# Kernel optimization log

Hardware: AMD Instinct MI355X
Metric: run time of the kernel (lower is better)

Reference implementation:

```python
import jax, jax.numpy as jnp
import numpy as np

D_MODEL = 1024
N_HEADS = 16
D_KV = 64
B, S = 2, 2048


def setup_inputs() -> dict:
    key = jax.random.key(0)
    ks = jax.random.split(key, 7)
    scale = 1.0 / np.sqrt(D_MODEL)
    return {
        "query": jax.random.normal(ks[0], (B, S, D_MODEL), jnp.float32),
        "key": jax.random.normal(ks[1], (B, S, D_MODEL), jnp.float32),
        "value": jax.random.normal(ks[2], (B, S, D_MODEL), jnp.float32),
        "mask": jnp.zeros((B, 1, 1, S), jnp.float32),
        "Wq": jax.random.normal(ks[3], (D_MODEL, N_HEADS * D_KV), jnp.float32) * scale,
        "Wk": jax.random.normal(ks[4], (D_MODEL, N_HEADS * D_KV), jnp.float32) * scale,
        "Wv": jax.random.normal(ks[5], (D_MODEL, N_HEADS * D_KV), jnp.float32) * scale,
        "Wo": jax.random.normal(ks[6], (N_HEADS * D_KV, D_MODEL), jnp.float32) * scale,
    }


def _split_heads(x):
    b, s, _ = x.shape
    return x.reshape(b, s, N_HEADS, D_KV).transpose(0, 2, 1, 3)  # [B,H,S,Dk]


def reference(query, key, value, mask, Wq, Wk, Wv, Wo):
    q = _split_heads(query @ Wq)
    k = _split_heads(key @ Wk)
    v = _split_heads(value @ Wv)
    scores = jnp.einsum("bhqd,bhkd->bhqk", q, k) / jnp.sqrt(
        jnp.asarray(D_KV, scores_dtype := q.dtype)
    )
    scores = scores + mask
    attn = jax.nn.softmax(scores, axis=-1)  # dropout_rate=0 -> identity
    ctx = jnp.einsum("bhqk,bhkd->bhqd", attn, v)
    ctx = ctx.transpose(0, 2, 1, 3).reshape(query.shape[0], -1, N_HEADS * D_KV)
    hidden = ctx @ Wo
    return hidden
```

## Files before the change

### kernel.cpp

```cpp
#include <hip/hip_runtime.h>
#include <hip/hip_bf16.h>
#include <stdint.h>

typedef __bf16 bf16;
typedef __bf16 bf16x8 __attribute__((ext_vector_type(8)));
typedef __bf16 bf16x4 __attribute__((ext_vector_type(4)));
typedef float  f32x4  __attribute__((ext_vector_type(4)));
typedef float  f32x16 __attribute__((ext_vector_type(16)));

#define S_LEN  2048
#define NH     16
#define DKV    64
#define DMODEL 1024
#define LOG2E  1.4426950408889634f

#define SBAR()       __builtin_amdgcn_s_barrier()
#define SFENCE()     __builtin_amdgcn_sched_barrier(0)
#define WAIT_VM(N)   asm volatile("s_waitcnt vmcnt(" #N ")" ::: "memory")
#define WAIT_LGKM0() asm volatile("s_waitcnt lgkmcnt(0)" ::: "memory")

__device__ __forceinline__ void async_load16(const void* g, void* l) {
  __builtin_amdgcn_global_load_lds(
      (const __attribute__((address_space(1))) uint32_t*)(uintptr_t)g,
      (__attribute__((address_space(3))) uint32_t*)(uintptr_t)l,
      16, 0, 0);
}

__global__ void transpose_w(const float* __restrict__ W0, const float* __restrict__ W1,
                            const float* __restrict__ W2, const float* __restrict__ W3,
                            bf16* __restrict__ T0, bf16* __restrict__ T1,
                            bf16* __restrict__ T2, bf16* __restrict__ T3)
{
  int z = blockIdx.z;
  const float* W = (z == 0) ? W0 : (z == 1) ? W1 : (z == 2) ? W2 : W3;
  bf16* T = (z == 0) ? T0 : (z == 1) ? T1 : (z == 2) ? T2 : T3;
  __shared__ float tile[64][65];
  int n0 = blockIdx.x * 64, k0 = blockIdx.y * 64;
  int tid = threadIdx.x;

  int c4 = (tid & 15) * 4;
  int rr = tid >> 4;
  for (int g = 0; g < 4; ++g) {
    int k = g * 16 + rr;
    f32x4 v = *(const f32x4*)(W + (size_t)(k0 + k) * DMODEL + n0 + c4);
    tile[k][c4] = v[0]; tile[k][c4 + 1] = v[1];
    tile[k][c4 + 2] = v[2]; tile[k][c4 + 3] = v[3];
  }
  __syncthreads();

  int kc = tid & 7, rn2 = tid >> 3;
  for (int pass = 0; pass < 2; ++pass) {
    int rn = pass * 32 + rn2;
    bf16x8 o;
    for (int w = 0; w < 8; ++w) o[w] = (bf16)tile[kc * 8 + w][rn];
    *(bf16x8*)(T + (size_t)(n0 + rn) * DMODEL + k0 + kc * 8) = o;
  }
}

__global__ __launch_bounds__(256) void gemm_qkv(
    const float* __restrict__ Aq, const float* __restrict__ Ak, const float* __restrict__ Av,
    const bf16* __restrict__ Bq, const bf16* __restrict__ Bk, const bf16* __restrict__ Bv,
    bf16* __restrict__ Cq, bf16* __restrict__ Ck, bf16* __restrict__ Cv)
{
  __shared__ __align__(16) char smem[49152];
  bf16* As  = (bf16*)smem;
  bf16* Bs0 = (bf16*)(smem + 16384);
  bf16* Bs1 = (bf16*)(smem + 32768);
  bf16* Ls  = (bf16*)smem;

  const int z = blockIdx.z;
  const float* A = (z == 0) ? Aq : (z == 1) ? Ak : Av;
  const bf16* Bt = (z == 0) ? Bq : (z == 1) ? Bk : Bv;
  bf16* C        = (z == 0) ? Cq : (z == 1) ? Ck : Cv;

  const int m0 = blockIdx.x * 128;
  const int n0 = blockIdx.y * 128;
  const int tid = threadIdx.x;
  const int lane = tid & 63;
  const int wave = tid >> 6;
  const int wm = (wave >> 1) * 64;
  const int wn = (wave & 1) * 64;
  const int row = lane & 15;
  const int quad = lane >> 4;

  f32x4 acc[4][4];
  for (int i = 0; i < 4; ++i)
    for (int j = 0; j < 4; ++j) acc[i][j] = (f32x4){0.f, 0.f, 0.f, 0.f};

  const int arc = tid & 7;
  const int arr = tid >> 3;
  const float* Ap0 = A + (size_t)(m0 +  0 + arr) * DMODEL + arc * 8;
  const float* Ap1 = A + (size_t)(m0 + 32 + arr) * DMODEL + arc * 8;
  const float* Ap2 = A + (size_t)(m0 + 64 + arr) * DMODEL + arc * 8;
  const float* Ap3 = A + (size_t)(m0 + 96 + arr) * DMODEL + arc * 8;

  auto stageB = [&](int kt, bf16* Bsel) {
    const int kk = kt << 6;
    for (int j = 0; j < 4; ++j) {
      int base = j * 256 + wave * 64;
      int idx = base + lane;
      int r = idx >> 3;
      int cc = (idx & 7) ^ (r & 7);
      async_load16(Bt + (size_t)(n0 + r) * DMODEL + kk + cc * 8,
                   (char*)Bsel + (size_t)base * 16);
    }
  };

  f32x4 av[4][2];
  av[0][0] = *(const f32x4*)(Ap0); av[0][1] = *(const f32x4*)(Ap0 + 4);
  av[1][0] = *(const f32x4*)(Ap1); av[1][1] = *(const f32x4*)(Ap1 + 4);
  av[2][0] = *(const f32x4*)(Ap2); av[2][1] = *(const f32x4*)(Ap2 + 4);
  av[3][0] = *(const f32x4*)(Ap3); av[3][1] = *(const f32x4*)(Ap3 + 4);
  SFENCE();
  stageB(0, Bs0);
  SFENCE();

  for (int kt = 0; kt < 16; ++kt) {
    bf16* Bcur = (kt & 1) ? Bs1 : Bs0;
    bf16* Bnxt = (kt & 1) ? Bs0 : Bs1;
    if (kt < 15) stageB(kt + 1, Bnxt);
#pragma unroll
    for (int g = 0; g < 4; ++g) {
      bf16x8 o;
      for (int w = 0; w < 4; ++w) { o[w] = (bf16)av[g][0][w]; o[w + 4] = (bf16)av[g][1][w]; }
      int r = g * 32 + arr;
      *(bf16x8*)(As + r * 64 + ((arc ^ (arr & 7)) << 3)) = o;
    }
    if (kt < 15) {
      const int kn = (kt + 1) << 6;
      av[0][0] = *(const f32x4*)(Ap0 + kn); av[0][1] = *(const f32x4*)(Ap0 + kn + 4);
      av[1][0] = *(const f32x4*)(Ap1 + kn); av[1][1] = *(const f32x4*)(Ap1 + kn + 4);
      av[2][0] = *(const f32x4*)(Ap2 + kn); av[2][1] = *(const f32x4*)(Ap2 + kn + 4);
      av[3][0] = *(const f32x4*)(Ap3 + kn); av[3][1] = *(const f32x4*)(Ap3 + kn + 4);
    }
    SFENCE();
    if (kt < 15) { WAIT_VM(12); }
    else         { WAIT_VM(0); }
    WAIT_LGKM0();
    SBAR();
    SFENCE();
    for (int ks = 0; ks < 2; ++ks) {
      bf16x8 af[4], bfr[4];
      for (int i = 0; i < 4; ++i) {
        int rr = wm + i * 16 + row;
        af[i] = *(const bf16x8*)(As + rr * 64 + (((quad + ks * 4) ^ (rr & 7)) << 3));
      }
      for (int j = 0; j < 4; ++j) {
        int rr = wn + j * 16 + row;
        bfr[j] = *(const bf16x8*)(Bcur + rr * 64 + (((quad + ks * 4) ^ (rr & 7)) << 3));
      }
      for (int i = 0; i < 4; ++i)
        for (int j = 0; j < 4; ++j)
          acc[i][j] = __builtin_amdgcn_mfma_f32_16x16x32_bf16(af[i], bfr[j], acc[i][j], 0, 0, 0);
    }
    SFENCE();
    SBAR();
  }

  if (z != 2) {
    const int bq = m0 >> 11;
    __syncthreads();
    for (int i = 0; i < 4; ++i)
      for (int j = 0; j < 4; ++j)
        for (int r = 0; r < 4; ++r)
          Ls[(wm + i * 16 + quad * 4 + r) * 132 + wn + j * 16 + row] = (bf16)acc[i][j][r];
    __syncthreads();
    for (int u = 0; u < 8; ++u) {
      int cc = u * 256 + tid;
      int rloc = cc >> 4, c8 = (cc & 15) * 8;
      int s = (m0 + rloc) & 2047;
      int gn = n0 + c8;
      int h = gn >> 6, d = gn & 63;
      bf16x8 val = *(const bf16x8*)(Ls + rloc * 132 + c8);
      *(bf16x8*)(C + (((size_t)(bq * NH + h)) * S_LEN + s) * DKV + d) = val;
    }
  } else {
    for (int i = 0; i < 4; ++i)
      for (int j = 0; j < 4; ++j) {
        int gm = m0 + wm + i * 16 + quad * 4;
        int gn = n0 + wn + j * 16 + row;
        int b = gm >> 11, s = gm & 2047;
        int h = gn >> 6,  d = gn & 63;
        int bh = b * NH + h;
        int tile = s >> 6, kb = (s & 63) >> 2;
        int half = (kb >> 1) & 1;
        int p = (kb & 1) + ((kb >> 2) & 1) * 2 + (kb >> 3) * 4;
        bf16x4 t;
        for (int r = 0; r < 4; ++r) t[r] = (bf16)acc[i][j][r];
        *(bf16x4*)(C + ((((size_t)bh * 32 + tile) * 8 + p) * 64 + d) * 8 + half * 4) = t;
      }
  }
}

__global__ __launch_bounds__(256, 4) void attn_kernel(
    const bf16* __restrict__ Qh, const bf16* __restrict__ Kh, const bf16* __restrict__ Vperm,
    const float* __restrict__ mask, bf16* __restrict__ Opart, float* __restrict__ Lpart)
{
  __shared__ __align__(16) bf16 Ks[2][64 * 64];
  __shared__ __align__(16) bf16 Vts[2][64 * 64];
  __shared__ __align__(16) float masks2[2][64];

  const int bh = blockIdx.x;
  const int b = bh >> 4;
  const int q0 = blockIdx.y * 128;
  const int zh = blockIdx.z;
  const int tid = threadIdx.x;
  const int lane = tid & 63;
  const int wave = tid >> 6;
  const int ln = lane & 31;
  const int hi = lane >> 5;
  const float SC2 = 0.125f * LOG2E;

  const int qg = q0 + wave * 32 + ln;
  bf16x8 qf[4];
  {
    const bf16* qrow = Qh + ((size_t)bh * S_LEN + qg) * DKV;
    for (int c = 0; c < 4; ++c)
      qf[c] = *(const bf16x8*)(qrow + c * 16 + hi * 8);
  }

  auto stage = [&](int it, int buf) {
    const int kv0 = zh * 1024 + it * 64;
    float mval = 0.f;
    if (tid < 64) mval = mask[b * S_LEN + kv0 + tid];
    const bf16* vtile = Vperm + ((size_t)bh * 32 + (kv0 >> 6)) * 4096;
    for (int j = 0; j < 2; ++j) {
      int base = j * 256 + wave * 64;
      int idx = base + lane;
      int r = idx >> 3;
      int cc = (idx & 7) ^ (r & 7);
      async_load16(Kh + ((size_t)bh * S_LEN + kv0 + r) * DKV + cc * 8,
                   (char*)Ks[buf] + (size_t)base * 16);
      async_load16(vtile + (size_t)idx * 8,
                   (char*)Vts[buf] + (size_t)base * 16);
    }
    if (tid < 64) masks2[buf][tid] = mval * LOG2E;
  };

  f32x16 O[2];
  for (int nb = 0; nb < 2; ++nb)
    for (int i = 0; i < 16; ++i) O[nb][i] = 0.f;
  float lsum = 0.f;

  stage(0, 0);

  for (int it = 0; it < 16; ++it) {
    const int cur = it & 1;
    if (it < 15) stage(it + 1, cur ^ 1);
    SFENCE();
    if (it < 15) { WAIT_VM(4); }
    else         { WAIT_VM(0); }
    WAIT_LGKM0();
    SBAR();
    SFENCE();

    f32x16 Sm[2];
    for (int i = 0; i < 16; ++i) { Sm[0][i] = 0.f; Sm[1][i] = 0.f; }
    for (int c = 0; c < 4; ++c) {
      bf16x8 k0 = *(const bf16x8*)(Ks[cur] + ln * 64        + (((2 * c + hi) ^ (ln & 7)) << 3));
      bf16x8 k1 = *(const bf16x8*)(Ks[cur] + (32 + ln) * 64 + (((2 * c + hi) ^ (ln & 7)) << 3));
      Sm[0] = __builtin_amdgcn_mfma_f32_32x32x16_bf16(k0, qf[c], Sm[0], 0, 0, 0);
      Sm[1] = __builtin_amdgcn_mfma_f32_32x32x16_bf16(k1, qf[c], Sm[1], 0, 0, 0);
    }

    for (int cg = 0; cg < 4; ++cg) {
      int mb = cg >> 1, g = cg & 1;
      int koff = 32 * mb + 16 * g + 4 * hi;
      f32x4 mklo = *(const f32x4*)(&masks2[cur][koff]);
      f32x4 mkhi = *(const f32x4*)(&masks2[cur][koff + 8]);
      bf16x8 ap;
      float ls0 = 0.f;
      for (int u = 0; u < 4; ++u) {
        float p = __builtin_amdgcn_exp2f(Sm[mb][g * 8 + u] * SC2 + mklo[u]);
        ls0 += p; ap[u] = (bf16)p;
      }
      for (int u = 0; u < 4; ++u) {
        float p = __builtin_amdgcn_exp2f(Sm[mb][g * 8 + 4 + u] * SC2 + mkhi[u]);
        ls0 += p; ap[4 + u] = (bf16)p;
      }
      lsum += ls0;
      int p = hi + 2 * g + 4 * mb;
      for (int nb = 0; nb < 2; ++nb) {
        int d = nb * 32 + ln;
        bf16x8 bv = *(const bf16x8*)(Vts[cur] + ((size_t)p * 64 + d) * 8);
        O[nb] = __builtin_amdgcn_mfma_f32_32x32x16_bf16(ap, bv, O[nb], 0, 0, 0);
      }
    }
    SFENCE();
    SBAR();
  }

  float lt = lsum + __shfl_xor(lsum, 32, 64);
  if (lane < 32)
    Lpart[((size_t)zh * 32 + bh) * S_LEN + q0 + wave * 32 + ln] = lt;

  bf16* ob = Opart + (((size_t)zh * 32 + bh) * S_LEN) * DKV;
  for (int g = 0; g < 4; ++g)
    for (int nb = 0; nb < 2; ++nb)
      for (int j = 0; j < 4; ++j) {
        int qrow = q0 + wave * 32 + j + 8 * g + 4 * hi;
        ob[(size_t)qrow * DKV + nb * 32 + ln] = (bf16)O[nb][g * 4 + j];
      }
}

__global__ __launch_bounds__(256) void gemm_out(
    const bf16* __restrict__ Opart, const float* __restrict__ Lpart,
    const bf16* __restrict__ Wot, float* __restrict__ Cout)
{
  __shared__ __align__(16) bf16 As[64 * 64];
  __shared__ __align__(16) bf16 Bs[2][128 * 64];
  __shared__ float rinv[NH * 64];

  const int m0 = blockIdx.x * 64;
  const int n0 = blockIdx.y * 128;
  const int tid = threadIdx.x;
  const int lane = tid & 63;
  const int wave = tid >> 6;
  const int wm = (wave >> 1) * 32;
  const int wn = (wave & 1) * 64;
  const int row = lane & 15;
  const int quad = lane >> 4;
  const int b = m0 >> 11;
  const int s0 = m0 & 2047;

  for (int u = 0; u < 4; ++u) {
    int idx = u * 256 + tid;
    int h = idx >> 6, r = idx & 63;
    float l = Lpart[(size_t)(b * NH + h) * S_LEN + s0 + r]
            + Lpart[(size_t)(32 + b * NH + h) * S_LEN + s0 + r];
    rinv[idx] = 1.0f / l;
  }
  SFENCE();

  f32x4 acc[2][4];
  for (int i = 0; i < 2; ++i)
    for (int j = 0; j < 4; ++j) acc[i][j] = (f32x4){0.f, 0.f, 0.f, 0.f};

  const int arc = tid & 7;
  const int arr = tid >> 3;
  const size_t HSTEP = (size_t)S_LEN * DKV;
  const size_t ZSTEP = (size_t)32 * S_LEN * DKV;
  const bf16* Oa = Opart + ((size_t)(b * NH) * S_LEN + s0 + arr) * DKV + arc * 8;
  const bf16* Ob = Oa + (size_t)32 * DKV;

  auto stageB = [&](int kt, int buf) {
    for (int j = 0; j < 4; ++j) {
      int base = j * 256 + wave * 64;
      int idx = base + lane;
      int r = idx >> 3;
      int cc = (idx & 7) ^ (r & 7);
      async_load16(Wot + (size_t)(n0 + r) * DMODEL + kt * 64 + cc * 8,
                   (char*)Bs[buf] + (size_t)base * 16);
    }
  };

  bf16x8 h00 = *(const bf16x8*)(Oa);
  bf16x8 h01 = *(const bf16x8*)(Oa + ZSTEP);
  bf16x8 h10 = *(const bf16x8*)(Ob);
  bf16x8 h11 = *(const bf16x8*)(Ob + ZSTEP);
  SFENCE();
  stageB(0, 0);
  SFENCE();
  WAIT_LGKM0();
  SBAR();

  for (int kt = 0; kt < 16; ++kt) {
    const int cur = kt & 1;
    if (kt < 15) stageB(kt + 1, cur ^ 1);
    {
      float rv  = rinv[kt * 64 + arr];
      float rv2 = rinv[kt * 64 + 32 + arr];
      bf16x8 o;
      for (int w = 0; w < 8; ++w)
        o[w] = (bf16)(((float)h00[w] + (float)h01[w]) * rv);
      *(bf16x8*)(As + arr * 64 + ((arc ^ (arr & 7)) << 3)) = o;
      for (int w = 0; w < 8; ++w)
        o[w] = (bf16)(((float)h10[w] + (float)h11[w]) * rv2);
      *(bf16x8*)(As + (32 + arr) * 64 + ((arc ^ (arr & 7)) << 3)) = o;
    }
    if (kt < 15) {
      const size_t off = (size_t)(kt + 1) * HSTEP;
      h00 = *(const bf16x8*)(Oa + off);
      h01 = *(const bf16x8*)(Oa + off + ZSTEP);
      h10 = *(const bf16x8*)(Ob + off);
      h11 = *(const bf16x8*)(Ob + off + ZSTEP);
    }
    SFENCE();
    if (kt < 15) { WAIT_VM(8); }
    else         { WAIT_VM(0); }
    WAIT_LGKM0();
    SBAR();
    SFENCE();
    for (int ks = 0; ks < 2; ++ks) {
      bf16x8 af[2], bfr[4];
      for (int i = 0; i < 2; ++i) {
        int rr = wm + i * 16 + row;
        af[i] = *(const bf16x8*)(As + rr * 64 + (((quad + ks * 4) ^ (rr & 7)) << 3));
      }
      for (int j = 0; j < 4; ++j) {
        int rr = wn + j * 16 + row;
        bfr[j] = *(const bf16x8*)(Bs[cur] + rr * 64 + (((quad + ks * 4) ^ (rr & 7)) << 3));
      }
      for (int i = 0; i < 2; ++i)
        for (int j = 0; j < 4; ++j)
          acc[i][j] = __builtin_amdgcn_mfma_f32_16x16x32_bf16(af[i], bfr[j], acc[i][j], 0, 0, 0);
    }
    SFENCE();
    SBAR();
  }

  for (int i = 0; i < 2; ++i)
    for (int j = 0; j < 4; ++j)
      for (int r = 0; r < 4; ++r) {
        int gm = m0 + wm + i * 16 + quad * 4 + r;
        int gn = n0 + wn + j * 16 + row;
        Cout[(size_t)gm * DMODEL + gn] = acc[i][j][r];
      }
}

extern "C" void kernel_launch(void* const* d_in, const int* in_sizes, int n_in,
                              void* d_out, int out_size, void* d_ws, size_t ws_size,
                              hipStream_t stream)
{
  const float* query = (const float*)d_in[0];
  const float* key_  = (const float*)d_in[1];
  const float* value = (const float*)d_in[2];
  const float* mask  = (const float*)d_in[3];
  const float* Wq = (const float*)d_in[4];
  const float* Wk = (const float*)d_in[5];
  const float* Wv = (const float*)d_in[6];
  const float* Wo = (const float*)d_in[7];

  char* ws = (char*)d_ws;
  const size_t MB = (size_t)1 << 20;
  bf16* qh    = (bf16*)(ws + 0 * MB);
  bf16* kh    = (bf16*)(ws + 8 * MB);
  bf16* vperm = (bf16*)(ws + 16 * MB);
  bf16* wot   = (bf16*)(ws + 24 * MB);
  bf16* Opart = (bf16*)(ws + 26 * MB);
  bf16* wqt   = (bf16*)(ws + 26 * MB);
  bf16* wkt   = (bf16*)(ws + 28 * MB);
  bf16* wvt   = (bf16*)(ws + 30 * MB);
  float* Lpart = (float*)(ws + 58 * MB);

  transpose_w<<<dim3(16, 16, 4), 256, 0, stream>>>(Wq, Wk, Wv, Wo, wqt, wkt, wvt, wot);
  gemm_qkv<<<dim3(32, 8, 3), 256, 0, stream>>>(query, key_, value, wqt, wkt, wvt,
                                               qh, kh, vperm);
  attn_kernel<<<dim3(32, 16, 2), 256, 0, stream>>>(qh, kh, vperm, mask, Opart, Lpart);
  gemm_out<<<dim3(64, 8), 256, 0, stream>>>(Opart, Lpart, wot, (float*)d_out);
}
```

Baseline: 209.6 us.

## Pre-convert QKV activations to bf16 in a fused prep kernel and simplify GEMM staging

The weight-transpose kernel now also converts the fp32 query/key/value activations to bf16 in a separate grid slice, writing them to new workspace buffers. The QKV GEMM then loads A tiles with async global-to-LDS copies like B, using a single LDS buffer with a full wait each k-step instead of double buffering B and converting fp32 A in registers. This removes the per-block fp32 A conversion and halves A read bytes inside the GEMM, but adds an extra activation round trip through memory and loses the load/compute overlap in the GEMM loop. Separately, s_setprio raises wave priority around the MFMA sections in the attention kernel.

```diff
diff --git a/kernel.cpp b/kernel.cpp
--- a/kernel.cpp
+++ b/kernel.cpp
@@ -26,50 +26,66 @@
       16, 0, 0);
 }
 
-__global__ void transpose_w(const float* __restrict__ W0, const float* __restrict__ W1,
-                            const float* __restrict__ W2, const float* __restrict__ W3,
-                            bf16* __restrict__ T0, bf16* __restrict__ T1,
-                            bf16* __restrict__ T2, bf16* __restrict__ T3)
+__global__ void prep(const float* __restrict__ W0, const float* __restrict__ W1,
+                     const float* __restrict__ W2, const float* __restrict__ W3,
+                     const float* __restrict__ Aq, const float* __restrict__ Ak,
+                     const float* __restrict__ Av,
+                     bf16* __restrict__ T0, bf16* __restrict__ T1,
+                     bf16* __restrict__ T2, bf16* __restrict__ T3,
+                     bf16* __restrict__ Qb, bf16* __restrict__ Kb, bf16* __restrict__ Vb)
 {
-  int z = blockIdx.z;
-  const float* W = (z == 0) ? W0 : (z == 1) ? W1 : (z == 2) ? W2 : W3;
-  bf16* T = (z == 0) ? T0 : (z == 1) ? T1 : (z == 2) ? T2 : T3;
-  __shared__ float tile[64][65];
-  int n0 = blockIdx.x * 64, k0 = blockIdx.y * 64;
-  int tid = threadIdx.x;
-
-  int c4 = (tid & 15) * 4;
-  int rr = tid >> 4;
-  for (int g = 0; g < 4; ++g) {
-    int k = g * 16 + rr;
-    f32x4 v = *(const f32x4*)(W + (size_t)(k0 + k) * DMODEL + n0 + c4);
-    tile[k][c4] = v[0]; tile[k][c4 + 1] = v[1];
-    tile[k][c4 + 2] = v[2]; tile[k][c4 + 3] = v[3];
-  }
-  __syncthreads();
-
-  int kc = tid & 7, rn2 = tid >> 3;
-  for (int pass = 0; pass < 2; ++pass) {
-    int rn = pass * 32 + rn2;
-    bf16x8 o;
-    for (int w = 0; w < 8; ++w) o[w] = (bf16)tile[kc * 8 + w][rn];
-    *(bf16x8*)(T + (size_t)(n0 + rn) * DMODEL + k0 + kc * 8) = o;
+  const int z = blockIdx.z;
+  const int tid = threadIdx.x;
+  if (z < 4) {
+    if (blockIdx.x >= 16) return;
+    const float* W = (z == 0) ? W0 : (z == 1) ? W1 : (z == 2) ? W2 : W3;
+    bf16* T = (z == 0) ? T0 : (z == 1) ? T1 : (z == 2) ? T2 : T3;
+    __shared__ float tile[64][65];
+    int n0 = blockIdx.x * 64, k0 = blockIdx.y * 64;
+    int c4 = (tid & 15) * 4;
+    int rr = tid >> 4;
+    for (int g = 0; g < 4; ++g) {
+      int k = g * 16 + rr;
+      f32x4 v = *(const f32x4*)(W + (size_t)(k0 + k) * DMODEL + n0 + c4);
+      tile[k][c4] = v[0]; tile[k][c4 + 1] = v[1];
+      tile[k][c4 + 2] = v[2]; tile[k][c4 + 3] = v[3];
+    }
+    __syncthreads();
+    int kc = tid & 7, rn2 = tid >> 3;
+    for (int pass = 0; pass < 2; ++pass) {
+      int rn = pass * 32 + rn2;
+      bf16x8 o;
+      for (int w = 0; w < 8; ++w) o[w] = (bf16)tile[kc * 8 + w][rn];
+      *(bf16x8*)(T + (size_t)(n0 + rn) * DMODEL + k0 + kc * 8) = o;
+    }
+  } else {
+    const float* S = (z == 4) ? Aq : (z == 5) ? Ak : Av;
+    bf16* D = (z == 4) ? Qb : (z == 5) ? Kb : Vb;
+    size_t base = (((size_t)blockIdx.y * 64 + blockIdx.x) * 256 + tid) * 16;
+    f32x4 v0 = *(const f32x4*)(S + base);
+    f32x4 v1 = *(const f32x4*)(S + base + 4);
+    f32x4 v2 = *(const f32x4*)(S + base + 8);
+    f32x4 v3 = *(const f32x4*)(S + base + 12);
+    bf16x8 o0, o1;
+    for (int w = 0; w < 4; ++w) { o0[w] = (bf16)v0[w]; o0[w + 4] = (bf16)v1[w]; }
+    for (int w = 0; w < 4; ++w) { o1[w] = (bf16)v2[w]; o1[w + 4] = (bf16)v3[w]; }
+    *(bf16x8*)(D + base) = o0;
+    *(bf16x8*)(D + base + 8) = o1;
   }
 }
 
 __global__ __launch_bounds__(256) void gemm_qkv(
-    const float* __restrict__ Aq, const float* __restrict__ Ak, const float* __restrict__ Av,
+    const bf16* __restrict__ Aq, const bf16* __restrict__ Ak, const bf16* __restrict__ Av,
     const bf16* __restrict__ Bq, const bf16* __restrict__ Bk, const bf16* __restrict__ Bv,
     bf16* __restrict__ Cq, bf16* __restrict__ Ck, bf16* __restrict__ Cv)
 {
-  __shared__ __align__(16) char smem[49152];
-  bf16* As  = (bf16*)smem;
-  bf16* Bs0 = (bf16*)(smem + 16384);
-  bf16* Bs1 = (bf16*)(smem + 32768);
-  bf16* Ls  = (bf16*)smem;
+  __shared__ __align__(16) char smem[33792];
+  bf16* As = (bf16*)smem;
+  bf16* Bs = (bf16*)(smem + 16384);
+  bf16* Ls = (bf16*)smem;
 
   const int z = blockIdx.z;
-  const float* A = (z == 0) ? Aq : (z == 1) ? Ak : Av;
+  const bf16* A  = (z == 0) ? Aq : (z == 1) ? Ak : Av;
   const bf16* Bt = (z == 0) ? Bq : (z == 1) ? Bk : Bv;
   bf16* C        = (z == 0) ? Cq : (z == 1) ? Ck : Cv;
 
@@ -87,58 +103,20 @@
   for (int i = 0; i < 4; ++i)
     for (int j = 0; j < 4; ++j) acc[i][j] = (f32x4){0.f, 0.f, 0.f, 0.f};
 
-  const int arc = tid & 7;
-  const int arr = tid >> 3;
-  const float* Ap0 = A + (size_t)(m0 +  0 + arr) * DMODEL + arc * 8;
-  const float* Ap1 = A + (size_t)(m0 + 32 + arr) * DMODEL + arc * 8;
-  const float* Ap2 = A + (size_t)(m0 + 64 + arr) * DMODEL + arc * 8;
-  const float* Ap3 = A + (size_t)(m0 + 96 + arr) * DMODEL + arc * 8;
-
-  auto stageB = [&](int kt, bf16* Bsel) {
+  for (int kt = 0; kt < 16; ++kt) {
     const int kk = kt << 6;
     for (int j = 0; j < 4; ++j) {
       int base = j * 256 + wave * 64;
       int idx = base + lane;
       int r = idx >> 3;
       int cc = (idx & 7) ^ (r & 7);
+      async_load16(A  + (size_t)(m0 + r) * DMODEL + kk + cc * 8,
+                   (char*)As + (size_t)base * 16);
       async_load16(Bt + (size_t)(n0 + r) * DMODEL + kk + cc * 8,
-                   (char*)Bsel + (size_t)base * 16);
-    }
-  };
-
-  f32x4 av[4][2];
-  av[0][0] = *(const f32x4*)(Ap0); av[0][1] = *(const f32x4*)(Ap0 + 4);
-  av[1][0] = *(const f32x4*)(Ap1); av[1][1] = *(const f32x4*)(Ap1 + 4);
-  av[2][0] = *(const f32x4*)(Ap2); av[2][1] = *(const f32x4*)(Ap2 + 4);
-  av[3][0] = *(const f32x4*)(Ap3); av[3][1] = *(const f32x4*)(Ap3 + 4);
-  SFENCE();
-  stageB(0, Bs0);
-  SFENCE();
-
-  for (int kt = 0; kt < 16; ++kt) {
-    bf16* Bcur = (kt & 1) ? Bs1 : Bs0;
-    bf16* Bnxt = (kt & 1) ? Bs0 : Bs1;
-    if (kt < 15) stageB(kt + 1, Bnxt);
-#pragma unroll
-    for (int g = 0; g < 4; ++g) {
-      bf16x8 o;
-      for (int w = 0; w < 4; ++w) { o[w] = (bf16)av[g][0][w]; o[w + 4] = (bf16)av[g][1][w]; }
-      int r = g * 32 + arr;
-      *(bf16x8*)(As + r * 64 + ((arc ^ (arr & 7)) << 3)) = o;
-    }
-    if (kt < 15) {
-      const int kn = (kt + 1) << 6;
-      av[0][0] = *(const f32x4*)(Ap0 + kn); av[0][1] = *(const f32x4*)(Ap0 + kn + 4);
-      av[1][0] = *(const f32x4*)(Ap1 + kn); av[1][1] = *(const f32x4*)(Ap1 + kn + 4);
-      av[2][0] = *(const f32x4*)(Ap2 + kn); av[2][1] = *(const f32x4*)(Ap2 + kn + 4);
-      av[3][0] = *(const f32x4*)(Ap3 + kn); av[3][1] = *(const f32x4*)(Ap3 + kn + 4);
-    }
-    SFENCE();
-    if (kt < 15) { WAIT_VM(12); }
-    else         { WAIT_VM(0); }
-    WAIT_LGKM0();
-    SBAR();
-    SFENCE();
+                   (char*)Bs + (size_t)base * 16);
+    }
+    WAIT_VM(0);
+    SBAR();
     for (int ks = 0; ks < 2; ++ks) {
       bf16x8 af[4], bfr[4];
       for (int i = 0; i < 4; ++i) {
@@ -147,13 +125,12 @@
       }
       for (int j = 0; j < 4; ++j) {
         int rr = wn + j * 16 + row;
-        bfr[j] = *(const bf16x8*)(Bcur + rr * 64 + (((quad + ks * 4) ^ (rr & 7)) << 3));
+        bfr[j] = *(const bf16x8*)(Bs + rr * 64 + (((quad + ks * 4) ^ (rr & 7)) << 3));
       }
       for (int i = 0; i < 4; ++i)
         for (int j = 0; j < 4; ++j)
           acc[i][j] = __builtin_amdgcn_mfma_f32_16x16x32_bf16(af[i], bfr[j], acc[i][j], 0, 0, 0);
     }
-    SFENCE();
     SBAR();
   }
 
@@ -256,12 +233,14 @@
 
     f32x16 Sm[2];
     for (int i = 0; i < 16; ++i) { Sm[0][i] = 0.f; Sm[1][i] = 0.f; }
+    __builtin_amdgcn_s_setprio(1);
     for (int c = 0; c < 4; ++c) {
       bf16x8 k0 = *(const bf16x8*)(Ks[cur] + ln * 64        + (((2 * c + hi) ^ (ln & 7)) << 3));
       bf16x8 k1 = *(const bf16x8*)(Ks[cur] + (32 + ln) * 64 + (((2 * c + hi) ^ (ln & 7)) << 3));
       Sm[0] = __builtin_amdgcn_mfma_f32_32x32x16_bf16(k0, qf[c], Sm[0], 0, 0, 0);
       Sm[1] = __builtin_amdgcn_mfma_f32_32x32x16_bf16(k1, qf[c], Sm[1], 0, 0, 0);
     }
+    __builtin_amdgcn_s_setprio(0);
 
     for (int cg = 0; cg < 4; ++cg) {
       int mb = cg >> 1, g = cg & 1;
@@ -280,11 +259,13 @@
       }
       lsum += ls0;
       int p = hi + 2 * g + 4 * mb;
+      __builtin_amdgcn_s_setprio(1);
       for (int nb = 0; nb < 2; ++nb) {
         int d = nb * 32 + ln;
         bf16x8 bv = *(const bf16x8*)(Vts[cur] + ((size_t)p * 64 + d) * 8);
         O[nb] = __builtin_amdgcn_mfma_f32_32x32x16_bf16(ap, bv, O[nb], 0, 0, 0);
       }
+      __builtin_amdgcn_s_setprio(0);
     }
     SFENCE();
     SBAR();
@@ -441,10 +422,14 @@
   bf16* wqt   = (bf16*)(ws + 26 * MB);
   bf16* wkt   = (bf16*)(ws + 28 * MB);
   bf16* wvt   = (bf16*)(ws + 30 * MB);
+  bf16* qb    = (bf16*)(ws + 32 * MB);
+  bf16* kb    = (bf16*)(ws + 40 * MB);
+  bf16* vb    = (bf16*)(ws + 48 * MB);
   float* Lpart = (float*)(ws + 58 * MB);
 
-  transpose_w<<<dim3(16, 16, 4), 256, 0, stream>>>(Wq, Wk, Wv, Wo, wqt, wkt, wvt, wot);
-  gemm_qkv<<<dim3(32, 8, 3), 256, 0, stream>>>(query, key_, value, wqt, wkt, wvt,
+  prep<<<dim3(64, 16, 7), 256, 0, stream>>>(Wq, Wk, Wv, Wo, query, key_, value,
+                                            wqt, wkt, wvt, wot, qb, kb, vb);
+  gemm_qkv<<<dim3(32, 8, 3), 256, 0, stream>>>(qb, kb, vb, wqt, wkt, wvt,
                                                qh, kh, vperm);
   attn_kernel<<<dim3(32, 16, 2), 256, 0, stream>>>(qh, kh, vperm, mask, Opart, Lpart);
   gemm_out<<<dim3(64, 8), 256, 0, stream>>>(Opart, Lpart, wot, (float*)d_out);
```

Result: slower. 218.2 us (+4.1%).
